# Performance work log

Hardware: AMD Instinct MI355X
Metric: run time of the kernel (lower is better)

The kernel has to match this reference:

```python
import jax, jax.numpy as jnp
import numpy as np

D_MODEL = 1024
N_HEADS = 16
D_HEAD = D_MODEL // N_HEADS
B, T = 2, 2048


def setup_inputs() -> dict:
    key = jax.random.key(0)
    ks = jax.random.split(key, 6)
    scale = 1.0 / np.sqrt(D_MODEL)
    x = jax.random.normal(ks[0], (B, T, D_MODEL), dtype=jnp.float32)
    mask = jax.random.randint(ks[1], (1, 1, T, T), 0, 2, dtype=jnp.int32)
    Wqkv = jax.random.normal(ks[2], (D_MODEL, 3 * D_MODEL), dtype=jnp.float32) * scale
    bqkv = jnp.zeros((3 * D_MODEL,), dtype=jnp.float32)
    Wproj = jax.random.normal(ks[3], (D_MODEL, D_MODEL), dtype=jnp.float32) * scale
    bproj = jnp.zeros((D_MODEL,), dtype=jnp.float32)
    return {"x": x, "mask": mask, "Wqkv": Wqkv, "bqkv": bqkv,
            "Wproj": Wproj, "bproj": bproj}


def reference(x, mask, Wqkv, bqkv, Wproj, bproj):
    Bx, Tx, C = x.shape
    qkv = x @ Wqkv + bqkv                      # [B,T,3C]
    q, k, v = jnp.split(qkv, 3, axis=-1)       # each [B,T,C]

    def heads(t):  # [B,T,C] -> [B,H,T,dh]
        return t.reshape(Bx, Tx, N_HEADS, D_HEAD).transpose(0, 2, 1, 3)

    q, k, v = heads(q), heads(k), heads(v)
    att = jnp.einsum('bhqd,bhkd->bhqk', q, k) / jnp.sqrt(jnp.float32(D_HEAD))
    att = jnp.where(mask == 1, -jnp.inf, att)
    att = jax.nn.softmax(att, axis=-1)
    out = jnp.einsum('bhqk,bhkd->bhqd', att, v)  # [B,H,T,dh]
    out = out.transpose(0, 2, 1, 3).reshape(Bx, Tx, C)
    return out @ Wproj + bproj
```

## Files before the change

kernel.cpp:

```cpp
#include <hip/hip_runtime.h>
#include <hip/hip_bf16.h>

#define T_DIM 2048
#define C_DIM 1024
#define NHEAD 16
#define DHEAD 64

typedef __attribute__((ext_vector_type(8))) short s16x8;
typedef __attribute__((ext_vector_type(4))) short s16x4;
typedef __attribute__((ext_vector_type(4))) float f32x4;
typedef __attribute__((ext_vector_type(4))) unsigned short u16x4;

typedef __attribute__((address_space(3))) unsigned short lds_us;
typedef const __attribute__((address_space(1))) void glb_v;

#define SC_QK (0.125f * 1.44269504f)

static __device__ __forceinline__ unsigned short f2bfu(float f){
  __hip_bfloat16 h = __float2bfloat16(f);
  unsigned short u;
  __builtin_memcpy(&u, &h, 2);
  return u;
}

static __device__ __forceinline__ unsigned cvt_pk_bf16(float lo, float hi){
  unsigned r;
  asm("v_cvt_pk_bf16_f32 %0, %1, %2" : "=v"(r) : "v"(lo), "v"(hi));
  return r;
}

static __device__ __forceinline__ f32x4 MFMA16(s16x8 a, s16x8 b, f32x4 c){
  return __builtin_amdgcn_mfma_f32_16x16x32_bf16(a, b, c, 0, 0, 0);
}

__global__ __launch_bounds__(256) void cvt_bf16_kernel(const float* __restrict__ in,
                                                       unsigned short* __restrict__ out, int n4){
  int i = blockIdx.x*256 + threadIdx.x;
  if (i < n4){
    float4 v = reinterpret_cast<const float4*>(in)[i];
    u16x4 o;
    o.x = f2bfu(v.x); o.y = f2bfu(v.y); o.z = f2bfu(v.z); o.w = f2bfu(v.w);
    reinterpret_cast<u16x4*>(out)[i] = o;
  }
}

__global__ __launch_bounds__(256) void transpose_cvt_kernel(const float* __restrict__ src,
                                                            unsigned short* __restrict__ dst,
                                                            int K, int N){
  __shared__ unsigned short tile[64][65];
  int n0 = blockIdx.x*64, k0 = blockIdx.y*64;
  int tid = threadIdx.x;
  #pragma unroll
  for (int i=0;i<16;i++){
    int e = i*256 + tid; int r = e>>6, c = e&63;
    tile[r][c] = f2bfu(src[(size_t)(k0+r)*N + n0 + c]);
  }
  __syncthreads();
  #pragma unroll
  for (int i=0;i<16;i++){
    int e = i*256 + tid; int r = e>>6, c = e&63;
    dst[(size_t)(n0+r)*K + k0 + c] = tile[c][r];
  }
}

__global__ __launch_bounds__(256) void mask_bits_kernel(const int* __restrict__ m,
                                                        unsigned int* __restrict__ bits){
  int i = blockIdx.x*256 + threadIdx.x;
  unsigned long long b = __ballot(m[i] == 1);
  int lane = threadIdx.x & 63;
  if (lane == 0)  bits[i>>5] = (unsigned int)b;
  if (lane == 32) bits[i>>5] = (unsigned int)(b>>32);
}

__global__ __launch_bounds__(256) void transpose_v_kernel(const unsigned short* __restrict__ v,
                                                          unsigned short* __restrict__ vt){
  __shared__ unsigned short tile[64][65];
  int bh = blockIdx.y;
  int t0 = blockIdx.x*64;
  const unsigned short* src = v + (size_t)bh*T_DIM*DHEAD;
  unsigned short* dst = vt + (size_t)bh*T_DIM*DHEAD;
  int tid = threadIdx.x;
  #pragma unroll
  for (int i=0;i<16;i++){
    int e = i*256+tid; int r = e>>6, c = e&63;
    tile[r][c] = src[(size_t)(t0+r)*DHEAD + c];
  }
  __syncthreads();
  #pragma unroll
  for (int i=0;i<16;i++){
    int e = i*256+tid; int r = e>>6, c = e&63;
    dst[(size_t)r*T_DIM + t0 + c] = tile[c][r];
  }
}

template<int MODE>
__global__ __launch_bounds__(256) void gemm_kernel(const unsigned short* __restrict__ A,
    const unsigned short* __restrict__ Bt, const float* __restrict__ bias,
    unsigned short* __restrict__ qo, unsigned short* __restrict__ ko,
    unsigned short* __restrict__ vo, float* __restrict__ out)
{
  const int K = 1024;
  __shared__ __align__(16) unsigned short As[128*64];
  __shared__ __align__(16) unsigned short Bs[128*64];
  int tid = threadIdx.x;
  int lane = tid & 63, wave = tid >> 6;
  int m0 = blockIdx.y*128, n0 = blockIdx.x*128;
  int wm = (wave>>1)*64, wn = (wave&1)*64;
  int lr = lane & 15, lg = lane >> 4;
  int srow  = wave*8 + (lane>>3);
  int sslot = (lane&7) ^ (lane>>3);
  const unsigned short* Asrc = A  + (size_t)(m0+srow)*K + sslot*8;
  const unsigned short* Bsrc = Bt + (size_t)(n0+srow)*K + sslot*8;
  unsigned ldsoff = (unsigned)(wave*512 + lane*8);
  f32x4 acc[4][4];
  #pragma unroll
  for (int i=0;i<4;i++){
    #pragma unroll
    for (int j=0;j<4;j++){
      #pragma unroll
      for (int r=0;r<4;r++) acc[i][j][r] = 0.f;
    }
  }
  for (int kt=0; kt<K; kt+=64){
    #pragma unroll
    for (int i=0;i<4;i++){
      __builtin_amdgcn_global_load_lds((glb_v*)(Asrc + (size_t)i*32*K + kt),
                                       (lds_us*)(As + ldsoff + i*2048), 16, 0, 0);
      __builtin_amdgcn_global_load_lds((glb_v*)(Bsrc + (size_t)i*32*K + kt),
                                       (lds_us*)(Bs + ldsoff + i*2048), 16, 0, 0);
    }
    __syncthreads();
    #pragma unroll
    for (int kk=0; kk<2; kk++){
      s16x8 av[4], bv[4];
      #pragma unroll
      for (int i=0;i<4;i++){
        av[i] = *reinterpret_cast<const s16x8*>(&As[(wm+i*16+lr)*64 + (((kk*4+lg)^(lr&7))<<3)]);
        bv[i] = *reinterpret_cast<const s16x8*>(&Bs[(wn+i*16+lr)*64 + (((kk*4+lg)^(lr&7))<<3)]);
      }
      #pragma unroll
      for (int i=0;i<4;i++){
        #pragma unroll
        for (int j=0;j<4;j++)
          acc[i][j] = MFMA16(av[i], bv[j], acc[i][j]);
      }
    }
    __syncthreads();
  }
  #pragma unroll
  for (int j=0;j<4;j++){
    int n = n0 + wn + j*16 + lr;
    float bvl = bias[n];
    #pragma unroll
    for (int i=0;i<4;i++){
      #pragma unroll
      for (int r=0;r<4;r++){
        int m = m0 + wm + i*16 + lg*4 + r;
        float val = acc[i][j][r] + bvl;
        if (MODE == 0){
          int which = n >> 10, c = n & 1023;
          int h = c >> 6, d = c & 63;
          int b = m >> 11, t = m & 2047;
          size_t idx = ((size_t)((b*NHEAD + h)*T_DIM + t))*DHEAD + d;
          if (which == 0)      qo[idx] = f2bfu(val * SC_QK);
          else if (which == 1) ko[idx] = f2bfu(val);
          else                 vo[idx] = f2bfu(val);
        } else {
          out[(size_t)m*C_DIM + n] = val;
        }
      }
    }
  }
}

__global__ __launch_bounds__(256) void attn_kernel(const unsigned short* __restrict__ q,
    const unsigned short* __restrict__ k, const unsigned short* __restrict__ vt,
    const unsigned int* __restrict__ mbits, unsigned short* __restrict__ aout)
{
  __shared__ __align__(16) unsigned short Ks[64*64];
  __shared__ __align__(16) unsigned short Vs[64*64];
  __shared__ __align__(16) unsigned short Ps[4][16][72];
  int bh = blockIdx.y;
  int q0 = blockIdx.x*64;
  int tid = threadIdx.x, lane = tid&63, wave = tid>>6;
  int lr = lane&15, lg = lane>>4;
  const unsigned short* qp = q  + (size_t)bh*T_DIM*DHEAD;
  const unsigned short* kp = k  + (size_t)bh*T_DIM*DHEAD;
  const unsigned short* vp = vt + (size_t)bh*T_DIM*DHEAD;
  int qw = q0 + wave*16;
  s16x8 qf[2];
  #pragma unroll
  for (int kk=0;kk<2;kk++)
    qf[kk] = *reinterpret_cast<const s16x8*>(qp + (size_t)(qw+lr)*DHEAD + kk*32 + lg*8);
  s16x8 ones;
  #pragma unroll
  for (int j=0;j<8;j++) ones[j] = (short)0x3F80;
  int srow  = wave*8 + (lane>>3);
  int sslot = (lane&7) ^ (lane>>3);
  const unsigned short* Ksrc = kp + (size_t)srow*DHEAD + sslot*8;
  const unsigned short* Vsrc = vp + (size_t)srow*T_DIM + sslot*8;
  unsigned ldsoff = (unsigned)(wave*512 + lane*8);
  f32x4 o[5];
  #pragma unroll
  for (int cb=0;cb<5;cb++){
    #pragma unroll
    for (int r=0;r<4;r++) o[cb][r]=0.f;
  }
  float m = -1e30f;
  const unsigned int* mptr = mbits + (size_t)(qw + lr)*(T_DIM/32);

  for (int k0=0; k0<T_DIM; k0+=64){
    #pragma unroll
    for (int i=0;i<2;i++){
      __builtin_amdgcn_global_load_lds((glb_v*)(Ksrc + (size_t)(k0 + i*32)*DHEAD),
                                       (lds_us*)(Ks + ldsoff + i*2048), 16, 0, 0);
      __builtin_amdgcn_global_load_lds((glb_v*)(Vsrc + (size_t)i*32*T_DIM + k0),
                                       (lds_us*)(Vs + ldsoff + i*2048), 16, 0, 0);
    }
    __syncthreads();
    f32x4 st[4];
    #pragma unroll
    for (int cb=0;cb<4;cb++){
      f32x4 a;
      #pragma unroll
      for (int r=0;r<4;r++) a[r]=0.f;
      #pragma unroll
      for (int kk=0;kk<2;kk++){
        s16x8 kf = *reinterpret_cast<const s16x8*>(
            &Ks[(cb*16+lr)*64 + (((kk*4+lg)^(lr&7))<<3)]);
        a = MFMA16(kf, qf[kk], a);
      }
      st[cb] = a;
    }
    unsigned mw0 = mptr[(k0>>5)];
    unsigned mw1 = mptr[(k0>>5)+1];
    #pragma unroll
    for (int cb=0;cb<4;cb++){
      unsigned msel = (cb<2) ? mw0 : mw1;
      unsigned ms = msel >> ((cb&1)*16 + lg*4);
      #pragma unroll
      for (int r=0;r<4;r++)
        st[cb][r] = ((ms>>r)&1u) ? -1e30f : st[cb][r];
    }
    float pmax = st[0][0];
    #pragma unroll
    for (int cb=0;cb<4;cb++){
      #pragma unroll
      for (int r=0;r<4;r++) pmax = fmaxf(pmax, st[cb][r]);
    }
    pmax = fmaxf(pmax, __shfl_xor(pmax, 16));
    pmax = fmaxf(pmax, __shfl_xor(pmax, 32));
    if (!__all(pmax <= m + 8.0f)){
      float mnew = fmaxf(m, pmax);
      float corr = exp2f(m - mnew);
      m = mnew;
      float corrO[4];
      #pragma unroll
      for (int r=0;r<4;r++) corrO[r] = __shfl(corr, lg*4 + r);
      #pragma unroll
      for (int cb=0;cb<5;cb++){
        #pragma unroll
        for (int r=0;r<4;r++) o[cb][r] *= corrO[r];
      }
    }
    #pragma unroll
    for (int cb=0;cb<4;cb++){
      #pragma unroll
      for (int r=0;r<4;r++) st[cb][r] = exp2f(st[cb][r] - m);
    }
    #pragma unroll
    for (int cb=0;cb<4;cb++){
      uint2 w;
      w.x = cvt_pk_bf16(st[cb][0], st[cb][1]);
      w.y = cvt_pk_bf16(st[cb][2], st[cb][3]);
      *reinterpret_cast<uint2*>(&Ps[wave][lr][cb*16 + lg*4]) = w;
    }
    s16x8 pf[2];
    #pragma unroll
    for (int kk=0;kk<2;kk++)
      pf[kk] = *reinterpret_cast<const s16x8*>(&Ps[wave][lr][kk*32 + lg*8]);
    #pragma unroll
    for (int cb=0;cb<4;cb++){
      #pragma unroll
      for (int kk=0;kk<2;kk++){
        s16x8 vf = *reinterpret_cast<const s16x8*>(
            &Vs[(cb*16+lr)*64 + (((kk*4+lg)^(lr&7))<<3)]);
        o[cb] = MFMA16(pf[kk], vf, o[cb]);
      }
    }
    o[4] = MFMA16(pf[0], ones, o[4]);
    o[4] = MFMA16(pf[1], ones, o[4]);
    __syncthreads();
  }
  int b = bh >> 4, h = bh & 15;
  #pragma unroll
  for (int r=0;r<4;r++){
    float l = o[4][r];
    float invO = l > 0.f ? 1.f/l : 0.f;
    int row = b*T_DIM + qw + lg*4 + r;
    #pragma unroll
    for (int cb=0;cb<4;cb++){
      int d = cb*16 + lr;
      aout[(size_t)row*C_DIM + h*DHEAD + d] = f2bfu(o[cb][r]*invO);
    }
  }
}

extern "C" void kernel_launch(void* const* d_in, const int* in_sizes, int n_in,
                              void* d_out, int out_size, void* d_ws, size_t ws_size,
                              hipStream_t stream){
  const float* x     = (const float*)d_in[0];
  const int*   mask  = (const int*)d_in[1];
  const float* Wqkv  = (const float*)d_in[2];
  const float* bqkv  = (const float*)d_in[3];
  const float* Wproj = (const float*)d_in[4];
  const float* bproj = (const float*)d_in[5];
  float* out = (float*)d_out;
  char* ws = (char*)d_ws;
  const size_t MB = (size_t)1<<20;
  unsigned short* xb     = (unsigned short*)(ws + 0*MB);
  unsigned short* wqkvT  = (unsigned short*)(ws + 8*MB);
  unsigned short* wprojT = (unsigned short*)(ws + 14*MB);
  unsigned int*   mbits  = (unsigned int*)(ws + 16*MB);
  unsigned short* qb     = (unsigned short*)(ws + 17*MB);
  unsigned short* kb     = (unsigned short*)(ws + 25*MB);
  unsigned short* vb     = (unsigned short*)(ws + 33*MB);
  unsigned short* vtb    = (unsigned short*)(ws + 41*MB);
  unsigned short* aout   = xb;

  cvt_bf16_kernel<<<dim3(4096), dim3(256), 0, stream>>>(x, xb, (2*2048*1024)/4);
  transpose_cvt_kernel<<<dim3(48,16), dim3(256), 0, stream>>>(Wqkv, wqkvT, 1024, 3072);
  transpose_cvt_kernel<<<dim3(16,16), dim3(256), 0, stream>>>(Wproj, wprojT, 1024, 1024);
  mask_bits_kernel<<<dim3((2048*2048)/256), dim3(256), 0, stream>>>(mask, mbits);
  gemm_kernel<0><<<dim3(24,32), dim3(256), 0, stream>>>(xb, wqkvT, bqkv, qb, kb, vb, nullptr);
  transpose_v_kernel<<<dim3(32,32), dim3(256), 0, stream>>>(vb, vtb);
  attn_kernel<<<dim3(32,32), dim3(256), 0, stream>>>(qb, kb, vtb, mbits, aout);
  gemm_kernel<1><<<dim3(8,32), dim3(256), 0, stream>>>(aout, wprojT, bproj, nullptr, nullptr, nullptr, out);
}
```

Before: 254.0 us.

## Double-buffer K/V tiles in LDS and prefetch next tile during compute

```diff
diff --git a/kernel.cpp b/kernel.cpp
--- a/kernel.cpp
+++ b/kernel.cpp
@@ -177,8 +177,8 @@
     const unsigned short* __restrict__ k, const unsigned short* __restrict__ vt,
     const unsigned int* __restrict__ mbits, unsigned short* __restrict__ aout)
 {
-  __shared__ __align__(16) unsigned short Ks[64*64];
-  __shared__ __align__(16) unsigned short Vs[64*64];
+  __shared__ __align__(16) unsigned short Ks[2][64*64];
+  __shared__ __align__(16) unsigned short Vs[2][64*64];
   __shared__ __align__(16) unsigned short Ps[4][16][72];
   int bh = blockIdx.y;
   int q0 = blockIdx.x*64;
@@ -200,6 +200,16 @@
   const unsigned short* Ksrc = kp + (size_t)srow*DHEAD + sslot*8;
   const unsigned short* Vsrc = vp + (size_t)srow*T_DIM + sslot*8;
   unsigned ldsoff = (unsigned)(wave*512 + lane*8);
+
+  #define STAGE_KV(buf, kbase)                                                        \
+    _Pragma("unroll")                                                                 \
+    for (int i=0;i<2;i++){                                                            \
+      __builtin_amdgcn_global_load_lds((glb_v*)(Ksrc + (size_t)((kbase) + i*32)*DHEAD),\
+                                       (lds_us*)(&Ks[buf][0] + ldsoff + i*2048), 16, 0, 0);\
+      __builtin_amdgcn_global_load_lds((glb_v*)(Vsrc + (size_t)i*32*T_DIM + (kbase)), \
+                                       (lds_us*)(&Vs[buf][0] + ldsoff + i*2048), 16, 0, 0);\
+    }
+
   f32x4 o[5];
   #pragma unroll
   for (int cb=0;cb<5;cb++){
@@ -209,15 +219,16 @@
   float m = -1e30f;
   const unsigned int* mptr = mbits + (size_t)(qw + lr)*(T_DIM/32);
 
-  for (int k0=0; k0<T_DIM; k0+=64){
-    #pragma unroll
-    for (int i=0;i<2;i++){
-      __builtin_amdgcn_global_load_lds((glb_v*)(Ksrc + (size_t)(k0 + i*32)*DHEAD),
-                                       (lds_us*)(Ks + ldsoff + i*2048), 16, 0, 0);
-      __builtin_amdgcn_global_load_lds((glb_v*)(Vsrc + (size_t)i*32*T_DIM + k0),
-                                       (lds_us*)(Vs + ldsoff + i*2048), 16, 0, 0);
-    }
-    __syncthreads();
+  STAGE_KV(0, 0);
+  unsigned mw0 = mptr[0], mw1 = mptr[1];
+  __syncthreads();
+
+  const int NT = T_DIM/64;
+  for (int t=0; t<NT; ++t){
+    int cur = t & 1;
+    if (t < NT-1) STAGE_KV(cur^1, (t+1)*64);
+    unsigned nmw0=0, nmw1=0;
+    if (t < NT-1){ nmw0 = mptr[2*t+2]; nmw1 = mptr[2*t+3]; }
     f32x4 st[4];
     #pragma unroll
     for (int cb=0;cb<4;cb++){
@@ -227,13 +238,11 @@
       #pragma unroll
       for (int kk=0;kk<2;kk++){
         s16x8 kf = *reinterpret_cast<const s16x8*>(
-            &Ks[(cb*16+lr)*64 + (((kk*4+lg)^(lr&7))<<3)]);
+            &Ks[cur][(cb*16+lr)*64 + (((kk*4+lg)^(lr&7))<<3)]);
         a = MFMA16(kf, qf[kk], a);
       }
       st[cb] = a;
     }
-    unsigned mw0 = mptr[(k0>>5)];
-    unsigned mw1 = mptr[(k0>>5)+1];
     #pragma unroll
     for (int cb=0;cb<4;cb++){
       unsigned msel = (cb<2) ? mw0 : mw1;
@@ -284,14 +293,16 @@
       #pragma unroll
       for (int kk=0;kk<2;kk++){
         s16x8 vf = *reinterpret_cast<const s16x8*>(
-            &Vs[(cb*16+lr)*64 + (((kk*4+lg)^(lr&7))<<3)]);
+            &Vs[cur][(cb*16+lr)*64 + (((kk*4+lg)^(lr&7))<<3)]);
         o[cb] = MFMA16(pf[kk], vf, o[cb]);
       }
     }
     o[4] = MFMA16(pf[0], ones, o[4]);
     o[4] = MFMA16(pf[1], ones, o[4]);
+    mw0 = nmw0; mw1 = nmw1;
     __syncthreads();
   }
+  #undef STAGE_KV
   int b = bh >> 4, h = bh & 15;
   #pragma unroll
   for (int r=0;r<4;r++){
```

New measurement: 260.6 us. 2.6% more time.

## Write V transposed from QKV GEMM epilogue and shrink projection GEMM M-tile

Applied to the files above, without the earlier changes.

```diff
diff --git a/kernel.cpp b/kernel.cpp
--- a/kernel.cpp
+++ b/kernel.cpp
@@ -72,49 +72,29 @@
   if (lane == 32) bits[i>>5] = (unsigned int)(b>>32);
 }
 
-__global__ __launch_bounds__(256) void transpose_v_kernel(const unsigned short* __restrict__ v,
-                                                          unsigned short* __restrict__ vt){
-  __shared__ unsigned short tile[64][65];
-  int bh = blockIdx.y;
-  int t0 = blockIdx.x*64;
-  const unsigned short* src = v + (size_t)bh*T_DIM*DHEAD;
-  unsigned short* dst = vt + (size_t)bh*T_DIM*DHEAD;
-  int tid = threadIdx.x;
-  #pragma unroll
-  for (int i=0;i<16;i++){
-    int e = i*256+tid; int r = e>>6, c = e&63;
-    tile[r][c] = src[(size_t)(t0+r)*DHEAD + c];
-  }
-  __syncthreads();
-  #pragma unroll
-  for (int i=0;i<16;i++){
-    int e = i*256+tid; int r = e>>6, c = e&63;
-    dst[(size_t)r*T_DIM + t0 + c] = tile[c][r];
-  }
-}
-
-template<int MODE>
+template<int MODE, int BM>
 __global__ __launch_bounds__(256) void gemm_kernel(const unsigned short* __restrict__ A,
     const unsigned short* __restrict__ Bt, const float* __restrict__ bias,
     unsigned short* __restrict__ qo, unsigned short* __restrict__ ko,
     unsigned short* __restrict__ vo, float* __restrict__ out)
 {
   const int K = 1024;
-  __shared__ __align__(16) unsigned short As[128*64];
+  const int FR = BM/32;
+  __shared__ __align__(16) unsigned short As[BM*64];
   __shared__ __align__(16) unsigned short Bs[128*64];
   int tid = threadIdx.x;
   int lane = tid & 63, wave = tid >> 6;
-  int m0 = blockIdx.y*128, n0 = blockIdx.x*128;
-  int wm = (wave>>1)*64, wn = (wave&1)*64;
+  int m0 = blockIdx.y*BM, n0 = blockIdx.x*128;
+  int wm = (wave>>1)*(BM/2), wn = (wave&1)*64;
   int lr = lane & 15, lg = lane >> 4;
   int srow  = wave*8 + (lane>>3);
   int sslot = (lane&7) ^ (lane>>3);
   const unsigned short* Asrc = A  + (size_t)(m0+srow)*K + sslot*8;
   const unsigned short* Bsrc = Bt + (size_t)(n0+srow)*K + sslot*8;
   unsigned ldsoff = (unsigned)(wave*512 + lane*8);
-  f32x4 acc[4][4];
-  #pragma unroll
-  for (int i=0;i<4;i++){
+  f32x4 acc[FR][4];
+  #pragma unroll
+  for (int i=0;i<FR;i++){
     #pragma unroll
     for (int j=0;j<4;j++){
       #pragma unroll
@@ -123,23 +103,25 @@
   }
   for (int kt=0; kt<K; kt+=64){
     #pragma unroll
-    for (int i=0;i<4;i++){
+    for (int i=0;i<FR;i++)
       __builtin_amdgcn_global_load_lds((glb_v*)(Asrc + (size_t)i*32*K + kt),
                                        (lds_us*)(As + ldsoff + i*2048), 16, 0, 0);
+    #pragma unroll
+    for (int i=0;i<4;i++)
       __builtin_amdgcn_global_load_lds((glb_v*)(Bsrc + (size_t)i*32*K + kt),
                                        (lds_us*)(Bs + ldsoff + i*2048), 16, 0, 0);
-    }
     __syncthreads();
     #pragma unroll
     for (int kk=0; kk<2; kk++){
-      s16x8 av[4], bv[4];
-      #pragma unroll
-      for (int i=0;i<4;i++){
+      s16x8 av[FR], bv[4];
+      #pragma unroll
+      for (int i=0;i<FR;i++)
         av[i] = *reinterpret_cast<const s16x8*>(&As[(wm+i*16+lr)*64 + (((kk*4+lg)^(lr&7))<<3)]);
+      #pragma unroll
+      for (int i=0;i<4;i++)
         bv[i] = *reinterpret_cast<const s16x8*>(&Bs[(wn+i*16+lr)*64 + (((kk*4+lg)^(lr&7))<<3)]);
-      }
-      #pragma unroll
-      for (int i=0;i<4;i++){
+      #pragma unroll
+      for (int i=0;i<FR;i++){
         #pragma unroll
         for (int j=0;j<4;j++)
           acc[i][j] = MFMA16(av[i], bv[j], acc[i][j]);
@@ -152,7 +134,7 @@
     int n = n0 + wn + j*16 + lr;
     float bvl = bias[n];
     #pragma unroll
-    for (int i=0;i<4;i++){
+    for (int i=0;i<FR;i++){
       #pragma unroll
       for (int r=0;r<4;r++){
         int m = m0 + wm + i*16 + lg*4 + r;
@@ -161,10 +143,16 @@
           int which = n >> 10, c = n & 1023;
           int h = c >> 6, d = c & 63;
           int b = m >> 11, t = m & 2047;
-          size_t idx = ((size_t)((b*NHEAD + h)*T_DIM + t))*DHEAD + d;
-          if (which == 0)      qo[idx] = f2bfu(val * SC_QK);
-          else if (which == 1) ko[idx] = f2bfu(val);
-          else                 vo[idx] = f2bfu(val);
+          if (which == 0){
+            size_t idx = ((size_t)((b*NHEAD + h)*T_DIM + t))*DHEAD + d;
+            qo[idx] = f2bfu(val * SC_QK);
+          } else if (which == 1){
+            size_t idx = ((size_t)((b*NHEAD + h)*T_DIM + t))*DHEAD + d;
+            ko[idx] = f2bfu(val);
+          } else {
+            size_t idx = ((size_t)((b*NHEAD + h)*DHEAD + d))*T_DIM + t;
+            vo[idx] = f2bfu(val);
+          }
         } else {
           out[(size_t)m*C_DIM + n] = val;
         }
@@ -324,7 +312,6 @@
   unsigned int*   mbits  = (unsigned int*)(ws + 16*MB);
   unsigned short* qb     = (unsigned short*)(ws + 17*MB);
   unsigned short* kb     = (unsigned short*)(ws + 25*MB);
-  unsigned short* vb     = (unsigned short*)(ws + 33*MB);
   unsigned short* vtb    = (unsigned short*)(ws + 41*MB);
   unsigned short* aout   = xb;
 
@@ -332,8 +319,7 @@
   transpose_cvt_kernel<<<dim3(48,16), dim3(256), 0, stream>>>(Wqkv, wqkvT, 1024, 3072);
   transpose_cvt_kernel<<<dim3(16,16), dim3(256), 0, stream>>>(Wproj, wprojT, 1024, 1024);
   mask_bits_kernel<<<dim3((2048*2048)/256), dim3(256), 0, stream>>>(mask, mbits);
-  gemm_kernel<0><<<dim3(24,32), dim3(256), 0, stream>>>(xb, wqkvT, bqkv, qb, kb, vb, nullptr);
-  transpose_v_kernel<<<dim3(32,32), dim3(256), 0, stream>>>(vb, vtb);
+  gemm_kernel<0,128><<<dim3(24,32), dim3(256), 0, stream>>>(xb, wqkvT, bqkv, qb, kb, vtb, nullptr);
   attn_kernel<<<dim3(32,32), dim3(256), 0, stream>>>(qb, kb, vtb, mbits, aout);
-  gemm_kernel<1><<<dim3(8,32), dim3(256), 0, stream>>>(aout, wprojT, bproj, nullptr, nullptr, nullptr, out);
-}
+  gemm_kernel<1,64><<<dim3(8,64), dim3(256), 0, stream>>>(aout, wprojT, bproj, nullptr, nullptr, nullptr, out);
+}
```

After: 257.3 us. No clear change (+1.3%).
